# Performance work log

Hardware: AMD Instinct MI355X
Metric: run time of the kernel (lower is better)

The kernel has to match this reference:

```python
import jax, jax.numpy as jnp
import numpy as np


def _ln(x, g, b, eps=1e-5):
    m = x.mean(-1, keepdims=True)
    v = ((x - m) ** 2).mean(-1, keepdims=True)
    return (x - m) / jnp.sqrt(v + eps) * g + b


def setup_inputs() -> dict:
    key = jax.random.key(0)
    ks = jax.random.split(key, 10)
    B, S, D, H, hd, C = 2, 2048, 1024, 16, 64, 16
    def rn(k, shape, s=0.02):
        return jax.random.normal(k, shape, jnp.float32) * s
    return dict(
        x=jax.random.normal(ks[0], (B, S, D), jnp.float32),
        chaos_features=jax.random.normal(ks[1], (C,), jnp.float32),
        ln_pre_g=jnp.ones(D, jnp.float32), ln_pre_b=jnp.zeros(D, jnp.float32),
        Wqkv=rn(ks[2], (3 * D, D)), bqkv=jnp.zeros(3 * D, jnp.float32),
        enc_W1=rn(ks[3], (D, C)), enc_b1=jnp.zeros(D, jnp.float32),
        enc_g1=jnp.ones(D, jnp.float32), enc_bb1=jnp.zeros(D, jnp.float32),
        enc_W2=rn(ks[4], (D, D)), enc_b2=jnp.zeros(D, jnp.float32),
        enc_g2=jnp.ones(D, jnp.float32), enc_bb2=jnp.zeros(D, jnp.float32),
        Wga=rn(ks[5], (H, C)), bga=jnp.zeros(H, jnp.float32),
        Wgv=rn(ks[6], (H, C)), bgv=jnp.zeros(H, jnp.float32),
        Wt=rn(ks[7], (1, C)), bt=jnp.zeros(1, jnp.float32),
        qrot=rn(ks[8], (H, hd, hd), 0.1),
        fscales=jnp.full((H,), 0.5, jnp.float32),
        Wout=rn(ks[9], (D, D)), bout=jnp.zeros(D, jnp.float32),
        ln_post_g=jnp.ones(D, jnp.float32), ln_post_b=jnp.zeros(D, jnp.float32),
    )


def reference(x, chaos_features, ln_pre_g, ln_pre_b, Wqkv, bqkv,
              enc_W1, enc_b1, enc_g1, enc_bb1, enc_W2, enc_b2, enc_g2, enc_bb2,
              Wga, bga, Wgv, bgv, Wt, bt, qrot, fscales, Wout, bout,
              ln_post_g, ln_post_b):
    B, S, D = x.shape
    H = qrot.shape[0]
    hd = D // H
    xn = _ln(x, ln_pre_g, ln_pre_b)
    qkv = (xn @ Wqkv.T + bqkv).reshape(B, S, 3, H, hd).transpose(2, 0, 3, 1, 4)
    q, k, v = qkv[0], qkv[1], qkv[2]  # each [B,H,S,hd]
    scores = jnp.einsum('bhqd,bhkd->bhqk', q, k) / jnp.sqrt(jnp.float32(hd))
    cf = chaos_features
    # chaos encoder: Linear->LN->ReLU->Linear->LN (dropout is eval no-op)
    h1 = jax.nn.relu(_ln(cf @ enc_W1.T + enc_b1, enc_g1, enc_bb1))
    ce = _ln(h1 @ enc_W2.T + enc_b2, enc_g2, enc_bb2).reshape(H, hd)
    gate_a = jax.nn.sigmoid(cf @ Wga.T + bga)  # [H]
    gate_v = jax.nn.sigmoid(cf @ Wgv.T + bgv)  # [H]
    temp = jax.nn.softplus(cf @ Wt.T + bt)[0] + 1.0
    # torch: matmul broadcast makes [H,H,hd]; flatten[:H*hd] keeps rotation 0 / scale 0 only
    sc = (ce @ qrot[0]) * jax.nn.sigmoid(fscales[0])  # [H,hd]
    bias_h = sc.sum(-1)  # [H], per-head scalar attention bias
    scores = (scores * gate_a[None, :, None, None] + bias_h[None, :, None, None]) / temp
    v = v + (sc * gate_v[:, None])[None, :, None, :]
    w = jax.nn.softmax(scores, axis=-1)
    att = jnp.einsum('bhqk,bhkd->bhqd', w, v).transpose(0, 2, 1, 3).reshape(B, S, D)
    out = att @ Wout.T + bout
    g = jax.nn.sigmoid(cf.mean()) * 0.5 + 0.5
    out = out * g + xn * (1.0 - g)
    return _ln(out, ln_post_g, ln_post_b), w
```

## Files before the change

kernel.cpp:

```cpp
#include <hip/hip_runtime.h>

typedef unsigned short u16;
typedef unsigned int   u32;
typedef __bf16 bf16x8 __attribute__((ext_vector_type(8)));
typedef float  f32x4  __attribute__((ext_vector_type(4)));
typedef u16    u16x4  __attribute__((ext_vector_type(4)));

#define MFMA16(a,b,c) __builtin_amdgcn_mfma_f32_16x16x32_bf16((a),(b),(c),0,0,0)

__device__ __forceinline__ float b2f(u16 u){ union{u32 i; float f;} x; x.i = ((u32)u)<<16; return x.f; }
__device__ __forceinline__ u16 f2b(float f){ union{float f; u32 i;} x; x.f = f;
  u32 r = x.i + 0x7FFFu + ((x.i>>16)&1u); return (u16)(r>>16); }

__device__ __forceinline__ float wred_sum(float v){
  v += __shfl_xor(v,32); v += __shfl_xor(v,16); v += __shfl_xor(v,8);
  v += __shfl_xor(v,4);  v += __shfl_xor(v,2);  v += __shfl_xor(v,1);
  return v;
}

__global__ void detect(const u32* __restrict__ lpg, int* __restrict__ flag){
  if (threadIdx.x == 0) flag[0] = (lpg[0] == 0x3F800000u) ? 1 : 0;
}

struct CanonArgs {
  const void* src[26];
  int n[26];
  int off[26];
};

__global__ __launch_bounds__(256) void canonize(CanonArgs a, const int* __restrict__ flag,
                                                u16* __restrict__ dst){
  bool f32 = flag[0] != 0;
  int stride = gridDim.x * blockDim.x;
  int gid = blockIdx.x * blockDim.x + threadIdx.x;
  for (int t = 0; t < 26; t++){
    int n = a.n[t];
    u16* d = dst + a.off[t];
    if (f32){
      const float* s = (const float*)a.src[t];
      for (int i = gid; i < n; i += stride) d[i] = f2b(s[i]);
    } else {
      const u16* s = (const u16*)a.src[t];
      for (int i = gid; i < n; i += stride) d[i] = s[i];
    }
  }
}

__global__ __launch_bounds__(256) void chaos1(const u16* __restrict__ cf, const u16* __restrict__ W1,
    const u16* __restrict__ b1, const u16* __restrict__ g1, const u16* __restrict__ bb1,
    float* __restrict__ ch)
{
  __shared__ float cfd[16];
  __shared__ float red[8];
  int tid = threadIdx.x, lane = tid&63, wv = tid>>6;
  if (tid < 16) cfd[tid] = b2f(cf[tid]);
  __syncthreads();
  float v[4], s=0.f, sq=0.f;
  #pragma unroll
  for (int i=0;i<4;i++){
    int d = tid + i*256;
    float a = b2f(b1[d]);
    for (int c=0;c<16;c++) a += cfd[c]*b2f(W1[d*16+c]);
    v[i]=a; s+=a; sq+=a*a;
  }
  s = wred_sum(s); sq = wred_sum(sq);
  if (!lane){ red[wv]=s; red[4+wv]=sq; }
  __syncthreads();
  float S=red[0]+red[1]+red[2]+red[3], SQ=red[4]+red[5]+red[6]+red[7];
  float mean=S/1024.f, var=SQ/1024.f-mean*mean, rstd=rsqrtf(var+1e-5f);
  #pragma unroll
  for (int i=0;i<4;i++){
    int d = tid+i*256;
    float x = (v[i]-mean)*rstd*b2f(g1[d]) + b2f(bb1[d]);
    ch[1088+d] = fmaxf(x, 0.f);
  }
}

__global__ __launch_bounds__(256) void chaos2(const float* __restrict__ ch, const u16* __restrict__ W2,
    const u16* __restrict__ b2v, float* __restrict__ t2)
{
  int dd = blockIdx.x*4 + (threadIdx.x>>6);
  int lane = threadIdx.x & 63;
  const float* h1 = ch + 1088;
  float a = 0.f;
  for (int t=0;t<16;t++){
    int j = t*64 + lane;
    a += h1[j]*b2f(W2[(size_t)dd*1024 + j]);
  }
  a = wred_sum(a);
  if (!lane) t2[dd] = a + b2f(b2v[dd]);
}

__global__ __launch_bounds__(1024) void chaos3(const float* __restrict__ t2,
    const u16* __restrict__ g2, const u16* __restrict__ bb2, const u16* __restrict__ qrot,
    const u16* __restrict__ fsc, const u16* __restrict__ cf,
    const u16* __restrict__ Wga, const u16* __restrict__ bga,
    const u16* __restrict__ Wgv, const u16* __restrict__ bgv,
    const u16* __restrict__ Wt, const u16* __restrict__ bt, float* __restrict__ ch)
{
  __shared__ float red[32];
  __shared__ float ce[1024];
  __shared__ float scb[1024];
  __shared__ float gaa[16], gva[16];
  __shared__ float tg[2];
  int tid = threadIdx.x, lane = tid&63, wv = tid>>6;
  float x = t2[tid];
  float s = wred_sum(x), sq = wred_sum(x*x);
  if (!lane){ red[wv]=s; red[16+wv]=sq; }
  __syncthreads();
  if (tid==0){
    float S=0.f,SQ=0.f;
    for (int i=0;i<16;i++){ S+=red[i]; SQ+=red[16+i]; }
    float mean=S/1024.f;
    red[0]=mean; red[1]=rsqrtf(SQ/1024.f - mean*mean + 1e-5f);
  }
  if (tid < 16){
    float ga=b2f(bga[tid]), gv=b2f(bgv[tid]);
    for (int c=0;c<16;c++){
      float cc = b2f(cf[c]);
      ga += cc*b2f(Wga[tid*16+c]);
      gv += cc*b2f(Wgv[tid*16+c]);
    }
    gaa[tid] = 1.f/(1.f+expf(-ga));
    gva[tid] = 1.f/(1.f+expf(-gv));
  }
  if (tid==0){
    float t=b2f(bt[0]), mcf=0.f;
    for (int c=0;c<16;c++){ float cc=b2f(cf[c]); t += cc*b2f(Wt[c]); mcf += cc; }
    mcf *= (1.f/16.f);
    tg[0] = log1pf(expf(t)) + 1.0f;
    float g = (1.f/(1.f+expf(-mcf)))*0.5f + 0.5f;
    ch[48] = g; ch[49] = 1.0f - g;
    tg[1] = 1.f/(1.f+expf(-b2f(fsc[0])));
  }
  __syncthreads();
  float mean = red[0], rstd = red[1];
  ce[tid] = (x - mean)*rstd*b2f(g2[tid]) + b2f(bb2[tid]);
  __syncthreads();
  int hh = tid >> 6, dcol = tid & 63;
  float sv = 0.f;
  for (int k=0;k<64;k++) sv += ce[hh*64+k]*b2f(qrot[k*64+dcol]);
  sv *= tg[1];
  scb[tid] = sv;
  ch[64+tid] = sv * gva[hh];
  __syncthreads();
  if (tid < 16){
    float bhsum=0.f;
    for (int d=0;d<64;d++) bhsum += scb[tid*64+d];
    float temp = tg[0];
    ch[tid]    = gaa[tid]*0.125f/temp;
    ch[16+tid] = bhsum/temp;
  }
}

template<int OUT_DYN>
__global__ __launch_bounds__(256) void ln_rows(const u16* __restrict__ in,
    const u16* __restrict__ gg, const u16* __restrict__ bb, void* __restrict__ out,
    const int* __restrict__ flag)
{
  __shared__ float red[8];
  int row = blockIdx.x, tid = threadIdx.x;
  int lane = tid & 63, wv = tid >> 6;
  u16x4 raw = *(const u16x4*)(in + (size_t)row*1024 + tid*4);
  float v[4];
  #pragma unroll
  for (int i=0;i<4;i++) v[i] = b2f(raw[i]);
  float s = v[0]+v[1]+v[2]+v[3];
  float sq = v[0]*v[0]+v[1]*v[1]+v[2]*v[2]+v[3]*v[3];
  s = wred_sum(s); sq = wred_sum(sq);
  if (!lane){ red[wv]=s; red[4+wv]=sq; }
  __syncthreads();
  float S=red[0]+red[1]+red[2]+red[3], SQ=red[4]+red[5]+red[6]+red[7];
  float mean = S*(1.0f/1024.0f);
  float var  = SQ*(1.0f/1024.0f) - mean*mean;
  float rstd = rsqrtf(var + 1e-5f);
  u16x4 og = *(const u16x4*)(gg + tid*4);
  u16x4 ob = *(const u16x4*)(bb + tid*4);
  float o[4];
  #pragma unroll
  for (int i=0;i<4;i++) o[i] = (v[i]-mean)*rstd*b2f(og[i]) + b2f(ob[i]);
  bool of32 = (OUT_DYN == 1) && (flag[0] != 0);
  if (of32){
    f32x4 of = {o[0], o[1], o[2], o[3]};
    *(f32x4*)((float*)out + (size_t)row*1024 + tid*4) = of;
  } else {
    u16x4 ob16;
    #pragma unroll
    for (int i=0;i<4;i++) ob16[i] = f2b(o[i]);
    *(u16x4*)((u16*)out + (size_t)row*1024 + tid*4) = ob16;
  }
}

template<int MODE>
__global__ __launch_bounds__(256) void gemm_nt(const u16* __restrict__ A,
    const u16* __restrict__ W, const u16* __restrict__ bias,
    const float* __restrict__ ch, u16* __restrict__ o0, u16* __restrict__ o1,
    u16* __restrict__ o2, const u16* __restrict__ xn, int Nt)
{
  __shared__ u16 Al[128*72];
  __shared__ u16 Bl[128*72];
  int tid = threadIdx.x;
  int bx = blockIdx.x % Nt, by = blockIdx.x / Nt;
  int lane = tid & 63, wv = tid >> 6;
  int wm = (wv >> 1)*64, wn = (wv & 1)*64;
  int l16 = lane & 15, l8 = (lane >> 4)*8;
  f32x4 acc[4][4] = {};
  const u16* Ag = A + (size_t)by*128*1024;
  const u16* Wg = W + (size_t)bx*128*1024;
  for (int k0=0;k0<1024;k0+=64){
    __syncthreads();
    #pragma unroll
    for (int i=0;i<4;i++){
      int c = tid + i*256, row = c>>3, col = (c&7)*8;
      *(bf16x8*)&Al[row*72+col] = *(const bf16x8*)&Ag[(size_t)row*1024 + k0 + col];
      *(bf16x8*)&Bl[row*72+col] = *(const bf16x8*)&Wg[(size_t)row*1024 + k0 + col];
    }
    __syncthreads();
    #pragma unroll
    for (int ks=0;ks<2;ks++){
      bf16x8 af[4], bfr[4];
      #pragma unroll
      for (int mi=0;mi<4;mi++) af[mi]  = *(const bf16x8*)&Al[(wm+mi*16+l16)*72 + ks*32 + l8];
      #pragma unroll
      for (int ni=0;ni<4;ni++) bfr[ni] = *(const bf16x8*)&Bl[(wn+ni*16+l16)*72 + ks*32 + l8];
      #pragma unroll
      for (int mi=0;mi<4;mi++){
        #pragma unroll
        for (int ni=0;ni<4;ni++)
          acc[mi][ni] = MFMA16(af[mi], bfr[ni], acc[mi][ni]);
      }
    }
  }
  float g=0.f, omg=0.f;
  if (MODE==1){ g = ch[48]; omg = ch[49]; }
  #pragma unroll
  for (int mi=0;mi<4;mi++){
    #pragma unroll
    for (int ni=0;ni<4;ni++){
      int n = bx*128 + wn + ni*16 + l16;
      float bv = b2f(bias[n]);
      #pragma unroll
      for (int r=0;r<4;r++){
        int m = by*128 + wm + mi*16 + (lane>>4)*4 + r;
        float val = acc[mi][ni][r] + bv;
        if (MODE==0){
          int which = n>>10, hh=(n>>6)&15, dd=n&63;
          int bb = m>>11, s = m&2047;
          size_t qk = ((size_t)(bb*16+hh)*2048 + s)*64 + dd;
          if (which==0)      o0[qk] = f2b(val);
          else if (which==1) o1[qk] = f2b(val);
          else o2[((size_t)(bb*16+hh)*64 + dd)*2048 + s] = f2b(val + ch[64 + hh*64 + dd]);
        } else {
          size_t idx = (size_t)m*1024 + n;
          o0[idx] = f2b(val*g + omg*b2f(xn[idx]));
        }
      }
    }
  }
}

__global__ __launch_bounds__(256) void attn_fused(const u16* __restrict__ qb,
    const u16* __restrict__ kb, const u16* __restrict__ vtb,
    const float* __restrict__ ch, u16* __restrict__ wout_b, float* __restrict__ wout_f,
    const int* __restrict__ flag, u16* __restrict__ attb)
{
  __shared__ u16 qs [64*72];
  __shared__ u16 ksm[128*72];
  __shared__ u16 vsm[64*136];
  __shared__ u16 wsm[64*136];
  int tid = threadIdx.x;
  int bid = blockIdx.x;
  int qt = bid & 31, bh = bid >> 5;
  int b = bh >> 4, h = bh & 15;
  int lane = tid & 63, wv = tid >> 6;
  int l16 = lane & 15, l4 = lane >> 4;
  float alpha = ch[h], beta = ch[16+h];
  bool of32 = flag[0] != 0;

  const u16* qg = qb + ((size_t)bh*2048 + qt*64)*64;
  #pragma unroll
  for (int i=0;i<2;i++){
    int c = tid + i*256, row = c>>3, col = (c&7)*8;
    *(bf16x8*)&qs[row*72+col] = *(const bf16x8*)&qg[row*64+col];
  }
  __syncthreads();
  bf16x8 a0 = *(const bf16x8*)&qs[(wv*16+l16)*72 + l4*8];
  bf16x8 a1 = *(const bf16x8*)&qs[(wv*16+l16)*72 + 32 + l4*8];

  float m_run[4], l_run[4];
  #pragma unroll
  for (int r=0;r<4;r++){ m_run[r] = -1e30f; l_run[r] = 0.f; }

  const u16* kg = kb + (size_t)bh*2048*64;
  for (int kt=0; kt<16; ++kt){
    __syncthreads();
    #pragma unroll
    for (int i=0;i<4;i++){
      int c = tid + i*256, row = c>>3, col=(c&7)*8;
      *(bf16x8*)&ksm[row*72+col] = *(const bf16x8*)&kg[(size_t)(kt*128+row)*64 + col];
    }
    __syncthreads();
    f32x4 s[8];
    #pragma unroll
    for (int nt=0;nt<8;nt++){
      bf16x8 b0 = *(const bf16x8*)&ksm[(nt*16+l16)*72 + l4*8];
      bf16x8 b1 = *(const bf16x8*)&ksm[(nt*16+l16)*72 + 32 + l4*8];
      f32x4 z = {0.f,0.f,0.f,0.f};
      z = MFMA16(a0,b0,z);
      z = MFMA16(a1,b1,z);
      s[nt] = z;
    }
    #pragma unroll
    for (int r=0;r<4;r++){
      float pm = -1e30f;
      #pragma unroll
      for (int nt=0;nt<8;nt++){ float t = s[nt][r]*alpha + beta; s[nt][r] = t; pm = fmaxf(pm, t); }
      pm = fmaxf(pm, __shfl_xor(pm,1)); pm = fmaxf(pm, __shfl_xor(pm,2));
      pm = fmaxf(pm, __shfl_xor(pm,4)); pm = fmaxf(pm, __shfl_xor(pm,8));
      float mn = fmaxf(m_run[r], pm);
      float e = 0.f;
      #pragma unroll
      for (int nt=0;nt<8;nt++) e += __expf(s[nt][r]-mn);
      e += __shfl_xor(e,1); e += __shfl_xor(e,2); e += __shfl_xor(e,4); e += __shfl_xor(e,8);
      l_run[r] = l_run[r]*__expf(m_run[r]-mn) + e;
      m_run[r] = mn;
    }
  }
  float inv_l[4];
  #pragma unroll
  for (int r=0;r<4;r++) inv_l[r] = 1.0f / l_run[r];

  f32x4 oacc[4] = {};
  const u16* vg = vtb + (size_t)bh*64*2048;
  for (int kt=0; kt<16; ++kt){
    __syncthreads();
    #pragma unroll
    for (int i=0;i<4;i++){
      int c = tid + i*256, row = c>>3, col=(c&7)*8;
      *(bf16x8*)&ksm[row*72+col] = *(const bf16x8*)&kg[(size_t)(kt*128+row)*64 + col];
    }
    #pragma unroll
    for (int i=0;i<4;i++){
      int c = tid + i*256, dr = c>>4, kc = (c&15)*8;
      *(bf16x8*)&vsm[dr*136+kc] = *(const bf16x8*)&vg[(size_t)dr*2048 + kt*128 + kc];
    }
    __syncthreads();
    f32x4 s[8];
    #pragma unroll
    for (int nt=0;nt<8;nt++){
      bf16x8 b0 = *(const bf16x8*)&ksm[(nt*16+l16)*72 + l4*8];
      bf16x8 b1 = *(const bf16x8*)&ksm[(nt*16+l16)*72 + 32 + l4*8];
      f32x4 z = {0.f,0.f,0.f,0.f};
      z = MFMA16(a0,b0,z);
      z = MFMA16(a1,b1,z);
      s[nt] = z;
    }
    #pragma unroll
    for (int r=0;r<4;r++){
      int qrow = wv*16 + l4*4 + r;
      size_t wrow = ((size_t)bh*2048 + qt*64 + qrow)*2048 + (size_t)kt*128;
      #pragma unroll
      for (int nt=0;nt<8;nt++){
        float sa = s[nt][r]*alpha + beta;
        float wv_ = __expf(sa - m_run[r]) * inv_l[r];
        u16 wb = f2b(wv_);
        if (of32) wout_f[wrow + nt*16 + l16] = wv_;
        else      wout_b[wrow + nt*16 + l16] = wb;
        wsm[qrow*136 + nt*16 + l16] = wb;
      }
    }
    #pragma unroll
    for (int kv=0;kv<4;kv++){
      bf16x8 aw = *(const bf16x8*)&wsm[(wv*16+l16)*136 + kv*32 + l4*8];
      #pragma unroll
      for (int dn=0;dn<4;dn++){
        bf16x8 bvv = *(const bf16x8*)&vsm[(dn*16+l16)*136 + kv*32 + l4*8];
        oacc[dn] = MFMA16(aw, bvv, oacc[dn]);
      }
    }
  }
  #pragma unroll
  for (int r=0;r<4;r++){
    int t = qt*64 + wv*16 + l4*4 + r;
    size_t base = ((size_t)(b*2048 + t)*16 + h)*64;
    #pragma unroll
    for (int dn=0;dn<4;dn++)
      attb[base + dn*16 + l16] = f2b(oacc[dn][r]);
  }
}

extern "C" void kernel_launch(void* const* d_in, const int* in_sizes, int n_in,
                              void* d_out, int out_size, void* d_ws, size_t ws_size,
                              hipStream_t stream)
{
  char* wsb = (char*)d_ws;
  float* ch = (float*)wsb;
  int* flag = (int*)(wsb + 14336);
  u16* canon = (u16*)(wsb + 16384);

  const int C_X=0, C_WQKV=4194304, C_W2=7340032, C_WOUT=8388608, C_QROT=9437184,
            C_CF=9441280, C_LPG=9441296, C_LPB=9442320, C_BQKV=9443344,
            C_W1=9446416, C_EB1=9462800, C_EG1=9463824, C_EBB1=9464848,
            C_EB2=9465872, C_EG2=9466896, C_EBB2=9467920,
            C_WGA=9468944, C_BGA=9469200, C_WGV=9469216, C_BGV=9469472,
            C_WT=9469488, C_BT=9469504, C_FSC=9469520,
            C_BOUT=9469536, C_LQG=9470560, C_LQB=9471584;

  u16* main16 = (u16*)(wsb + 19922944);
  u16* xn   = main16;
  u16* qb   = xn   + 4194304;
  u16* kb   = qb   + 4194304;
  u16* vtb  = kb   + 4194304;
  u16* attb = vtb  + 4194304;
  u16* outb = qb;

  CanonArgs ca;
  const int ns[26]  = {4194304,16,1024,1024,3145728,3072,16384,1024,1024,1024,
                       1048576,1024,1024,1024,256,16,256,16,16,1,
                       4096,16,1048576,1024,1024,1024};
  const int offs[26]= {C_X,C_CF,C_LPG,C_LPB,C_WQKV,C_BQKV,C_W1,C_EB1,C_EG1,C_EBB1,
                       C_W2,C_EB2,C_EG2,C_EBB2,C_WGA,C_BGA,C_WGV,C_BGV,C_WT,C_BT,
                       C_QROT,C_FSC,C_WOUT,C_BOUT,C_LQG,C_LQB};
  for (int i=0;i<26;i++){ ca.src[i]=d_in[i]; ca.n[i]=ns[i]; ca.off[i]=offs[i]; }

  hipLaunchKernelGGL(detect, dim3(1), dim3(64), 0, stream, (const u32*)d_in[2], flag);
  hipLaunchKernelGGL(canonize, dim3(2048), dim3(256), 0, stream, ca, flag, canon);

  hipLaunchKernelGGL(chaos1, dim3(1),   dim3(256),  0, stream,
                     canon+C_CF, canon+C_W1, canon+C_EB1, canon+C_EG1, canon+C_EBB1, ch);
  hipLaunchKernelGGL(chaos2, dim3(256), dim3(256),  0, stream, ch, canon+C_W2, canon+C_EB2, ch+2112);
  hipLaunchKernelGGL(chaos3, dim3(1),   dim3(1024), 0, stream, ch+2112,
                     canon+C_EG2, canon+C_EBB2, canon+C_QROT, canon+C_FSC, canon+C_CF,
                     canon+C_WGA, canon+C_BGA, canon+C_WGV, canon+C_BGV,
                     canon+C_WT, canon+C_BT, ch);
  hipLaunchKernelGGL((ln_rows<0>), dim3(4096), dim3(256), 0, stream,
                     canon+C_X, canon+C_LPG, canon+C_LPB, (void*)xn, flag);
  hipLaunchKernelGGL((gemm_nt<0>), dim3(768), dim3(256), 0, stream,
                     xn, canon+C_WQKV, canon+C_BQKV, ch, qb, kb, vtb, (const u16*)nullptr, 24);

  u16*   wout_b = (u16*)d_out + 4194304;
  float* wout_f = (float*)d_out + 4194304;
  hipLaunchKernelGGL(attn_fused, dim3(1024), dim3(256), 0, stream,
                     qb, kb, vtb, ch, wout_b, wout_f, flag, attb);
  hipLaunchKernelGGL((gemm_nt<1>), dim3(256), dim3(256), 0, stream,
                     attb, canon+C_WOUT, canon+C_BOUT, ch, outb, (u16*)nullptr, (u16*)nullptr, xn, 8);
  hipLaunchKernelGGL((ln_rows<1>), dim3(4096), dim3(256), 0, stream,
                     outb, canon+C_LQG, canon+C_LQB, d_out, flag);
}
```

Baseline: 889.6 us.

## Vectorize canonize, use direct-to-LDS swizzled GEMM loads, coalesce attention weight stores

Canonize now converts and copies four elements per thread with vector loads and stores. The GEMM loads tiles straight into LDS with global_load_lds into an XOR-swizzled unpadded layout. The attention kernel stages softmax weights in shared memory and writes them to global memory as coalesced 4-wide rows, and it raises wave priority around the MFMA sections. The weight write is the largest output stream, so coalescing it targets the main memory cost. In f32 mode the stored weights are now rounded through bf16, which reduces output precision, and an extra barrier is added per tile.

```diff
diff --git a/kernel.cpp b/kernel.cpp
--- a/kernel.cpp
+++ b/kernel.cpp
@@ -16,6 +16,12 @@
   v += __shfl_xor(v,32); v += __shfl_xor(v,16); v += __shfl_xor(v,8);
   v += __shfl_xor(v,4);  v += __shfl_xor(v,2);  v += __shfl_xor(v,1);
   return v;
+}
+
+__device__ __forceinline__ void gload_lds16(const u16* g, u16* l){
+  __builtin_amdgcn_global_load_lds(
+      (const __attribute__((address_space(1))) void*)(const void*)g,
+      (__attribute__((address_space(3))) void*)(void*)l, 16, 0, 0);
 }
 
 __global__ void detect(const u32* __restrict__ lpg, int* __restrict__ flag){
@@ -35,13 +41,23 @@
   int gid = blockIdx.x * blockDim.x + threadIdx.x;
   for (int t = 0; t < 26; t++){
     int n = a.n[t];
+    int n4 = n >> 2;
     u16* d = dst + a.off[t];
     if (f32){
       const float* s = (const float*)a.src[t];
-      for (int i = gid; i < n; i += stride) d[i] = f2b(s[i]);
+      for (int i = gid; i < n4; i += stride){
+        f32x4 v = *(const f32x4*)(s + (size_t)i*4);
+        u16x4 o;
+        #pragma unroll
+        for (int j=0;j<4;j++) o[j] = f2b(v[j]);
+        *(u16x4*)(d + (size_t)i*4) = o;
+      }
+      if (gid < (n & 3)){ int i = (n & ~3) + gid; d[i] = f2b(s[i]); }
     } else {
       const u16* s = (const u16*)a.src[t];
-      for (int i = gid; i < n; i += stride) d[i] = s[i];
+      for (int i = gid; i < n4; i += stride)
+        *(u16x4*)(d + (size_t)i*4) = *(const u16x4*)(s + (size_t)i*4);
+      if (gid < (n & 3)){ int i = (n & ~3) + gid; d[i] = s[i]; }
     }
   }
 }
@@ -197,32 +213,44 @@
     const float* __restrict__ ch, u16* __restrict__ o0, u16* __restrict__ o1,
     u16* __restrict__ o2, const u16* __restrict__ xn, int Nt)
 {
-  __shared__ u16 Al[128*72];
-  __shared__ u16 Bl[128*72];
+  __shared__ u16 Al[128*64];
+  __shared__ u16 Bl[128*64];
   int tid = threadIdx.x;
   int bx = blockIdx.x % Nt, by = blockIdx.x / Nt;
   int lane = tid & 63, wv = tid >> 6;
   int wm = (wv >> 1)*64, wn = (wv & 1)*64;
-  int l16 = lane & 15, l8 = (lane >> 4)*8;
+  int l16 = lane & 15, l4v = lane >> 4;
   f32x4 acc[4][4] = {};
   const u16* Ag = A + (size_t)by*128*1024;
   const u16* Wg = W + (size_t)bx*128*1024;
+  int srow = lane >> 3;
+  int sseg = lane & 7;
   for (int k0=0;k0<1024;k0+=64){
     __syncthreads();
     #pragma unroll
     for (int i=0;i<4;i++){
-      int c = tid + i*256, row = c>>3, col = (c&7)*8;
-      *(bf16x8*)&Al[row*72+col] = *(const bf16x8*)&Ag[(size_t)row*1024 + k0 + col];
-      *(bf16x8*)&Bl[row*72+col] = *(const bf16x8*)&Wg[(size_t)row*1024 + k0 + col];
+      int r0 = wv*8 + i*32;
+      int row = r0 + srow;
+      int gseg = sseg ^ (row & 7);
+      gload_lds16(&Ag[(size_t)row*1024 + k0 + gseg*8], &Al[r0*64 + lane*8]);
+      gload_lds16(&Wg[(size_t)row*1024 + k0 + gseg*8], &Bl[r0*64 + lane*8]);
     }
     __syncthreads();
     #pragma unroll
     for (int ks=0;ks<2;ks++){
       bf16x8 af[4], bfr[4];
       #pragma unroll
-      for (int mi=0;mi<4;mi++) af[mi]  = *(const bf16x8*)&Al[(wm+mi*16+l16)*72 + ks*32 + l8];
-      #pragma unroll
-      for (int ni=0;ni<4;ni++) bfr[ni] = *(const bf16x8*)&Bl[(wn+ni*16+l16)*72 + ks*32 + l8];
+      for (int mi=0;mi<4;mi++){
+        int r = wm + mi*16 + l16;
+        int sg = (ks*4 + l4v) ^ (r & 7);
+        af[mi] = *(const bf16x8*)&Al[r*64 + sg*8];
+      }
+      #pragma unroll
+      for (int ni=0;ni<4;ni++){
+        int r = wn + ni*16 + l16;
+        int sg = (ks*4 + l4v) ^ (r & 7);
+        bfr[ni] = *(const bf16x8*)&Bl[r*64 + sg*8];
+      }
       #pragma unroll
       for (int mi=0;mi<4;mi++){
         #pragma unroll
@@ -301,6 +329,7 @@
     }
     __syncthreads();
     f32x4 s[8];
+    __builtin_amdgcn_s_setprio(1);
     #pragma unroll
     for (int nt=0;nt<8;nt++){
       bf16x8 b0 = *(const bf16x8*)&ksm[(nt*16+l16)*72 + l4*8];
@@ -310,6 +339,7 @@
       z = MFMA16(a1,b1,z);
       s[nt] = z;
     }
+    __builtin_amdgcn_s_setprio(0);
     #pragma unroll
     for (int r=0;r<4;r++){
       float pm = -1e30f;
@@ -346,6 +376,7 @@
     }
     __syncthreads();
     f32x4 s[8];
+    __builtin_amdgcn_s_setprio(1);
     #pragma unroll
     for (int nt=0;nt<8;nt++){
       bf16x8 b0 = *(const bf16x8*)&ksm[(nt*16+l16)*72 + l4*8];
@@ -355,20 +386,35 @@
       z = MFMA16(a1,b1,z);
       s[nt] = z;
     }
+    __builtin_amdgcn_s_setprio(0);
     #pragma unroll
     for (int r=0;r<4;r++){
       int qrow = wv*16 + l4*4 + r;
-      size_t wrow = ((size_t)bh*2048 + qt*64 + qrow)*2048 + (size_t)kt*128;
       #pragma unroll
       for (int nt=0;nt<8;nt++){
         float sa = s[nt][r]*alpha + beta;
         float wv_ = __expf(sa - m_run[r]) * inv_l[r];
-        u16 wb = f2b(wv_);
-        if (of32) wout_f[wrow + nt*16 + l16] = wv_;
-        else      wout_b[wrow + nt*16 + l16] = wb;
-        wsm[qrow*136 + nt*16 + l16] = wb;
-      }
-    }
+        wsm[qrow*136 + nt*16 + l16] = f2b(wv_);
+      }
+    }
+    __syncthreads();
+    {
+      int r2 = lane >> 5;
+      int c4 = (lane & 31) * 4;
+      #pragma unroll
+      for (int i=0;i<8;i++){
+        int row = wv*16 + i*2 + r2;
+        u16x4 wb4 = *(const u16x4*)&wsm[row*136 + c4];
+        size_t gidx = ((size_t)bh*2048 + qt*64 + row)*2048 + (size_t)kt*128 + c4;
+        if (of32){
+          f32x4 wf = {b2f(wb4[0]), b2f(wb4[1]), b2f(wb4[2]), b2f(wb4[3])};
+          *(f32x4*)(wout_f + gidx) = wf;
+        } else {
+          *(u16x4*)(wout_b + gidx) = wb4;
+        }
+      }
+    }
+    __builtin_amdgcn_s_setprio(1);
     #pragma unroll
     for (int kv=0;kv<4;kv++){
       bf16x8 aw = *(const bf16x8*)&wsm[(wv*16+l16)*136 + kv*32 + l4*8];
@@ -378,6 +424,7 @@
         oacc[dn] = MFMA16(aw, bvv, oacc[dn]);
       }
     }
+    __builtin_amdgcn_s_setprio(0);
   }
   #pragma unroll
   for (int r=0;r<4;r++){
```

Result: faster. 852.3 us (-4.2%).
